# Kernel tuning notes

Measured on AMD Instinct MI355X. Metric: run time of the kernel, lower is better.

Reference implementation:

```python
import jax, jax.numpy as jnp
import numpy as np

N_NODES = 100000
N_EDGES = 1600000
IN_CH = 64
HID = 64
N_LAYERS = 4


def setup_inputs() -> dict:
    key = jax.random.key(0)
    ks = jax.random.split(key, 12)
    x = jax.random.normal(ks[0], (N_NODES, IN_CH), dtype=jnp.float32)
    edge_index = jax.random.randint(ks[1], (2, N_EDGES), 0, N_NODES, dtype=jnp.int64)
    s = 1.0 / np.sqrt(HID)
    W_enc = jax.random.normal(ks[2], (IN_CH, HID), dtype=jnp.float32) * s
    b_enc = jnp.zeros((HID,), dtype=jnp.float32)
    Wg = jax.random.normal(ks[3], (N_LAYERS, HID, HID), dtype=jnp.float32) * s
    bg = jnp.zeros((N_LAYERS, HID), dtype=jnp.float32)
    # MLPReadout: 64 -> 32 -> 16 -> 1
    W0 = jax.random.normal(ks[4], (HID, HID // 2), dtype=jnp.float32) * s
    b0 = jnp.zeros((HID // 2,), dtype=jnp.float32)
    W1 = jax.random.normal(ks[5], (HID // 2, HID // 4), dtype=jnp.float32) * (1.0 / np.sqrt(HID // 2))
    b1 = jnp.zeros((HID // 4,), dtype=jnp.float32)
    W2 = jax.random.normal(ks[6], (HID // 4, 1), dtype=jnp.float32) * (1.0 / np.sqrt(HID // 4))
    b2 = jnp.zeros((1,), dtype=jnp.float32)
    return {"x": x, "edge_index": edge_index, "W_enc": W_enc, "b_enc": b_enc,
            "Wg": Wg, "bg": bg, "W0": W0, "b0": b0, "W1": W1, "b1": b1,
            "W2": W2, "b2": b2}


def _gcn_norm(edge_index, n_nodes):
    # PyG GCNConv default: add self-loops, symmetric normalization.
    loop = jnp.arange(n_nodes, dtype=edge_index.dtype)
    src = jnp.concatenate([edge_index[0], loop])  # [E + N]
    dst = jnp.concatenate([edge_index[1], loop])
    deg = jax.ops.segment_sum(jnp.ones_like(dst, dtype=jnp.float32), dst,
                              num_segments=n_nodes)
    dinv = jnp.where(deg > 0, 1.0 / jnp.sqrt(deg), 0.0)
    norm = dinv[src] * dinv[dst]  # [E + N]
    return src, dst, norm


def reference(x, edge_index, W_enc, b_enc, Wg, bg, W0, b0, W1, b1, W2, b2):
    n_nodes = x.shape[0]
    src, dst, norm = _gcn_norm(edge_index, n_nodes)
    h = x @ W_enc + b_enc  # feature encoder [N, HID]
    n_layers = Wg.shape[0]
    for l in range(n_layers):
        h_res = h
        hw = h @ Wg[l]                                  # [N, HID] GEMM
        msg = hw[src] * norm[:, None]                   # gather + scale
        h = jax.ops.segment_sum(msg, dst, num_segments=n_nodes) + bg[l]
        h = h + h_res                                   # residual
        if l != n_layers - 1:
            # dropout in eval mode is identity
            h = jax.nn.relu(h)
    # MLPReadout (L=2)
    y = jax.nn.relu(h @ W0 + b0)
    y = jax.nn.relu(y @ W1 + b1)
    y = y @ W2 + b2  # [N, 1]
    return y
```

## Files before the change

kernel.cpp:

```cpp
#include <hip/hip_runtime.h>

typedef __attribute__((ext_vector_type(8))) short bf16x8_t;
typedef __attribute__((ext_vector_type(4))) float f32x4_t;

#define PINF(x) asm volatile("" : "+v"(x))


#define PCHUNK 4096
#define PTHREADS 512
#define EPT (PCHUNK / PTHREADS)
#define NBUCK_MAX 400
#define BCAP 6144

__global__ __launch_bounds__(PTHREADS)
void k_partition2(const int* __restrict__ src, const int* __restrict__ dst,
                  int* __restrict__ bcnt, unsigned int* __restrict__ stageg,
                  int E, int nbuck) {
    __shared__ int hist[NBUCK_MAX];
    __shared__ int boffs[NBUCK_MAX];
    __shared__ int cur[NBUCK_MAX];
    __shared__ int gbase[NBUCK_MAX];
    __shared__ int tmp[PTHREADS];
    __shared__ unsigned int stage[PCHUNK];
    __shared__ unsigned short sbid[PCHUNK];

    int tid = threadIdx.x;
    int ebase = blockIdx.x * PCHUNK;
    int ecount = min(PCHUNK, E - ebase);

    if (tid < NBUCK_MAX) hist[tid] = 0;
    __syncthreads();

    int dreg[EPT], sreg[EPT];
#pragma unroll
    for (int k = 0; k < EPT; k++) {
        int e = ebase + tid + k * PTHREADS;
        if (tid + k * PTHREADS < ecount) {
            dreg[k] = dst[e];
            sreg[k] = src[e];
            atomicAdd(&hist[dreg[k] >> 8], 1);
        } else dreg[k] = -1;
    }
    __syncthreads();

    int v = (tid < nbuck) ? hist[tid] : 0;
    tmp[tid] = v;
    __syncthreads();
    for (int d = 1; d < PTHREADS; d <<= 1) {
        int t = (tid >= d) ? tmp[tid - d] : 0;
        __syncthreads();
        tmp[tid] += t;
        __syncthreads();
    }
    if (tid < nbuck) { boffs[tid] = tmp[tid] - v; cur[tid] = tmp[tid] - v; }
    __syncthreads();

#pragma unroll
    for (int k = 0; k < EPT; k++) {
        if (dreg[k] >= 0) {
            int b = dreg[k] >> 8;
            int p = atomicAdd(&cur[b], 1);
            stage[p] = ((unsigned int)(dreg[k] & 255) << 17) | (unsigned int)sreg[k];
            sbid[p] = (unsigned short)b;
        }
    }
    __syncthreads();

    if (tid < nbuck) {
        int c = cur[tid] - boffs[tid];
        if (c > 0) gbase[tid] = atomicAdd(&bcnt[tid], c);
    }
    __syncthreads();

    for (int i = tid; i < ecount; i += PTHREADS) {
        int b = sbid[i];
        stageg[(size_t)b * BCAP + gbase[b] + (i - boffs[b])] = stage[i];
    }
}


__global__ __launch_bounds__(512)
void k_bucket_scan(const int* __restrict__ bcnt, int* __restrict__ bbase, int nbuck) {
    __shared__ int tmp[512];
    int tid = threadIdx.x;
    int v = (tid < nbuck) ? bcnt[tid] : 0;
    tmp[tid] = v;
    __syncthreads();
    for (int d = 1; d < 512; d <<= 1) {
        int t = (tid >= d) ? tmp[tid - d] : 0;
        __syncthreads();
        tmp[tid] += t;
        __syncthreads();
    }
    if (tid < nbuck) bbase[tid] = tmp[tid] - v;
    if (tid == nbuck - 1) bbase[nbuck] = tmp[tid];
}


__global__ __launch_bounds__(1024)
void k_finefill2(const unsigned int* __restrict__ stageg, const int* __restrict__ bcnt,
                 const int* __restrict__ bbase, int* __restrict__ offs,
                 float* __restrict__ dinv, int* __restrict__ col, int N, int nbuck) {
    __shared__ int cnt0[256];
    __shared__ int excl[256];
    __shared__ int cur[256];
    __shared__ unsigned int stage[BCAP];
    int b = blockIdx.x;
    int tid = threadIdx.x;
    int nbase = b << 8;
    int nn = min(256, N - nbase);
    int n = bcnt[b];
    int base = bbase[b];
    const unsigned int* sg = stageg + (size_t)b * BCAP;

    if (tid < 256) cnt0[tid] = 0;
    __syncthreads();

    for (int i = tid; i < n; i += 1024)
        atomicAdd(&cnt0[sg[i] >> 17], 1);
    __syncthreads();

    if (tid < 256) excl[tid] = cnt0[tid];
    __syncthreads();
    for (int d = 1; d < 256; d <<= 1) {
        int t = 0;
        if (tid < 256 && tid >= d) t = excl[tid - d];
        __syncthreads();
        if (tid < 256) excl[tid] += t;
        __syncthreads();
    }
    if (tid < 256) {
        int e = excl[tid] - cnt0[tid];
        cur[tid] = e;
        if (tid < nn) {
            offs[nbase + tid] = base + e;
            dinv[nbase + tid] = rsqrtf((float)(cnt0[tid] + 1));
        }
    }
    if (b == nbuck - 1 && tid == 0) offs[N] = bbase[nbuck];
    __syncthreads();

    for (int i = tid; i < n; i += 1024) {
        unsigned int v = sg[i];
        int p = atomicAdd(&cur[v >> 17], 1);
        stage[p] = v & 0x1FFFFu;
    }
    __syncthreads();
    for (int i = tid; i < n; i += 1024)
        col[base + i] = (int)stage[i];
}


__device__ __forceinline__ unsigned int bf16rne(float x) {
    unsigned int u = __float_as_uint(x);
    return (u + 0x7FFFu + ((u >> 16) & 1u)) >> 16;
}
__device__ __forceinline__ float u2flo(unsigned int u) { return __uint_as_float(u << 16); }
__device__ __forceinline__ float u2fhi(unsigned int u) { return __uint_as_float(u & 0xFFFF0000u); }

__device__ __forceinline__ void split2(float a, float b, unsigned int& hi, unsigned int& lo) {
    unsigned int ha = bf16rne(a), hb = bf16rne(b);
    float ra = a - u2flo(ha), rb = b - u2flo(hb);
    hi = ha | (hb << 16);
    lo = bf16rne(ra) | (bf16rne(rb) << 16);
}

union FragU { uint4 u4; bf16x8_t bf; };


__global__ __launch_bounds__(256)
void k_wsplit(const float* __restrict__ Wenc, const float* __restrict__ Wg,
              unsigned int* __restrict__ wfragg, int* __restrict__ bcnt) {
    int m = blockIdx.x;
    int tid = threadIdx.x;
    if (m == 0 && tid < 256) { bcnt[tid] = 0; bcnt[tid + 256] = 0; }
    const float* W = (m == 0) ? Wenc : (Wg + (size_t)(m - 1) * 4096);
    unsigned int* wb = wfragg + (size_t)m * 4096;
#pragma unroll
    for (int i = 0; i < 16; i++) {
        int flat = tid * 16 + i;
        int mm = flat & 3;
        int l = (flat >> 2) & 63;
        int fp = flat >> 8;
        int p = fp & 1;
        int f = fp >> 1;
        int ct = f >> 1, kh = f & 1;
        int k = kh * 32 + ((l >> 4) << 3) + 2 * mm;
        int c = ct * 16 + (l & 15);
        float w0 = W[k * 64 + c];
        float w1 = W[(k + 1) * 64 + c];
        unsigned int hi, lo;
        split2(w0, w1, hi, lo);
        wb[flat] = p ? lo : hi;
    }
}


__global__ __launch_bounds__(256)
void k_enc_fused(const float* __restrict__ x, const uint4* __restrict__ wfE,
                 const float* __restrict__ benc, const uint4* __restrict__ wfG,
                 const float* __restrict__ dinv, float* __restrict__ h,
                 unsigned short* __restrict__ hwb_out, int N) {
    __shared__ float hlds[64 * 68];

    int tid = threadIdx.x;
    int lane = tid & 63;
    int w = tid >> 6;
    int rowbase = blockIdx.x * 64 + w * 16;

    FragU ahi[2], alo[2];
    {
        int row = rowbase + (lane & 15);
        int rc = min(row, N - 1);
#pragma unroll
        for (int kh = 0; kh < 2; kh++) {
            const float4* hp = (const float4*)(x + (size_t)rc * 64 + kh * 32 + ((lane >> 4) << 3));
            float4 p0 = hp[0], p1 = hp[1];
            split2(p0.x, p0.y, ahi[kh].u4.x, alo[kh].u4.x);
            split2(p0.z, p0.w, ahi[kh].u4.y, alo[kh].u4.y);
            split2(p1.x, p1.y, ahi[kh].u4.z, alo[kh].u4.z);
            split2(p1.z, p1.w, ahi[kh].u4.w, alo[kh].u4.w);
        }
    }

    f32x4_t acc[4];
#pragma unroll
    for (int ct = 0; ct < 4; ct++) {
        float b = benc[ct * 16 + (lane & 15)];
        acc[ct] = (f32x4_t){b, b, b, b};
    }
#pragma unroll
    for (int ct = 0; ct < 4; ct++) {
#pragma unroll
        for (int kh = 0; kh < 2; kh++) {
            FragU bhi, blo;
            bhi.u4 = wfE[((ct * 2 + kh) * 2 + 0) * 64 + lane];
            blo.u4 = wfE[((ct * 2 + kh) * 2 + 1) * 64 + lane];
            acc[ct] = __builtin_amdgcn_mfma_f32_16x16x32_bf16(ahi[kh].bf, bhi.bf, acc[ct], 0, 0, 0);
            acc[ct] = __builtin_amdgcn_mfma_f32_16x16x32_bf16(alo[kh].bf, bhi.bf, acc[ct], 0, 0, 0);
            acc[ct] = __builtin_amdgcn_mfma_f32_16x16x32_bf16(ahi[kh].bf, blo.bf, acc[ct], 0, 0, 0);
        }
    }

    float dv[4];
#pragma unroll
    for (int r = 0; r < 4; r++) {
        int row = rowbase + ((lane >> 4) << 2) + r;
        dv[r] = dinv[min(row, N - 1)];
    }
#pragma unroll
    for (int ct = 0; ct < 4; ct++) {
#pragma unroll
        for (int r = 0; r < 4; r++) {
            int row = rowbase + ((lane >> 4) << 2) + r;
            float v = acc[ct][r];
            if (row < N) h[(size_t)row * 64 + ct * 16 + (lane & 15)] = v;
            hlds[(w * 16 + ((lane >> 4) << 2) + r) * 68 + ct * 16 + (lane & 15)] = v * dv[r];
        }
    }
    __syncthreads();

    FragU a2hi[2], a2lo[2];
#pragma unroll
    for (int kh = 0; kh < 2; kh++) {
        const float4* hp = (const float4*)(hlds + (w * 16 + (lane & 15)) * 68 + kh * 32 + ((lane >> 4) << 3));
        float4 p0 = hp[0], p1 = hp[1];
        split2(p0.x, p0.y, a2hi[kh].u4.x, a2lo[kh].u4.x);
        split2(p0.z, p0.w, a2hi[kh].u4.y, a2lo[kh].u4.y);
        split2(p1.x, p1.y, a2hi[kh].u4.z, a2lo[kh].u4.z);
        split2(p1.z, p1.w, a2hi[kh].u4.w, a2lo[kh].u4.w);
    }

#pragma unroll
    for (int ct = 0; ct < 4; ct++) {
        f32x4_t a2 = (f32x4_t){0.f, 0.f, 0.f, 0.f};
#pragma unroll
        for (int kh = 0; kh < 2; kh++) {
            FragU bhi, blo;
            bhi.u4 = wfG[((ct * 2 + kh) * 2 + 0) * 64 + lane];
            blo.u4 = wfG[((ct * 2 + kh) * 2 + 1) * 64 + lane];
            a2 = __builtin_amdgcn_mfma_f32_16x16x32_bf16(a2hi[kh].bf, bhi.bf, a2, 0, 0, 0);
            a2 = __builtin_amdgcn_mfma_f32_16x16x32_bf16(a2lo[kh].bf, bhi.bf, a2, 0, 0, 0);
            a2 = __builtin_amdgcn_mfma_f32_16x16x32_bf16(a2hi[kh].bf, blo.bf, a2, 0, 0, 0);
        }
#pragma unroll
        for (int r = 0; r < 4; r++) {
            float v = a2[r];
            float vo = __shfl_xor(v, 1);
            int row = rowbase + ((lane >> 4) << 2) + r;
            if (!(lane & 1) && row < N) {
                unsigned int pk = bf16rne(v) | (bf16rne(vo) << 16);
                *(unsigned int*)(hwb_out + (size_t)row * 64 + ct * 16 + (lane & 15)) = pk;
            }
        }
    }
}


__global__ __launch_bounds__(256, 4)
void k_agg_fused(const unsigned short* __restrict__ hwb_in, const int* __restrict__ offs,
                 const int* __restrict__ col, const float* __restrict__ dinv,
                 const float* __restrict__ bg, float* __restrict__ h,
                 const uint4* __restrict__ wnext, unsigned short* __restrict__ hwb_out,
                 int N) {
    __shared__ uint4 wlds[16 * 64];

    int tid = threadIdx.x;
#pragma unroll
    for (int i = 0; i < 4; i++)
        wlds[tid + i * 256] = wnext[tid + i * 256];
    __syncthreads();

    int t = blockIdx.x * 256 + tid;
    int wid = t >> 6;
    int lane = tid & 63;
    int G = lane >> 3;
    int L = lane & 7;
    int node = wid * 8 + G;
    bool valid = node < N;
    int nc = valid ? node : N - 1;

    int start = offs[nc];
    int end = valid ? offs[nc + 1] : start;

    float dn = dinv[nc];
    float* hrow = h + (size_t)nc * 64 + L * 8;
    float4 hr0 = ((const float4*)hrow)[0];
    float4 hr1 = ((const float4*)hrow)[1];
    const float* bgp = bg + L * 8;
    float bs0 = bgp[0] + hr0.x, bs1 = bgp[1] + hr0.y, bs2 = bgp[2] + hr0.z, bs3 = bgp[3] + hr0.w;
    float bs4 = bgp[4] + hr1.x, bs5 = bgp[5] + hr1.y, bs6 = bgp[6] + hr1.z, bs7 = bgp[7] + hr1.w;
    PINF(bs0); PINF(bs1); PINF(bs2); PINF(bs3);
    PINF(bs4); PINF(bs5); PINF(bs6); PINF(bs7); PINF(dn);

    uint4 v = ((const uint4*)(hwb_in + (size_t)nc * 64))[L];
    float a0 = u2flo(v.x), a1 = u2fhi(v.x);
    float a2 = u2flo(v.y), a3 = u2fhi(v.y);
    float a4 = u2flo(v.z), a5 = u2fhi(v.z);
    float a6 = u2flo(v.w), a7 = u2fhi(v.w);

    int last = (end > start) ? (end - 1) : 0;
    int e = start;
    int cc0 = col[min(e + 0, last)];
    int cc1 = col[min(e + 1, last)];
    int cc2 = col[min(e + 2, last)];
    int cc3 = col[min(e + 3, last)];
    for (;;) {
        bool act0 = e < end;
        if (__ballot(act0) == 0ULL) break;
        bool act1 = e + 1 < end, act2 = e + 2 < end, act3 = e + 3 < end;
        uint4 v0 = ((const uint4*)(hwb_in + (size_t)cc0 * 64))[L];
        uint4 v1 = ((const uint4*)(hwb_in + (size_t)cc1 * 64))[L];
        uint4 v2 = ((const uint4*)(hwb_in + (size_t)cc2 * 64))[L];
        uint4 v3 = ((const uint4*)(hwb_in + (size_t)cc3 * 64))[L];
        int en = e + 4;
        cc0 = col[min(en + 0, last)];
        cc1 = col[min(en + 1, last)];
        cc2 = col[min(en + 2, last)];
        cc3 = col[min(en + 3, last)];
        if (!act0) { v0.x = 0u; v0.y = 0u; v0.z = 0u; v0.w = 0u; }
        if (!act1) { v1.x = 0u; v1.y = 0u; v1.z = 0u; v1.w = 0u; }
        if (!act2) { v2.x = 0u; v2.y = 0u; v2.z = 0u; v2.w = 0u; }
        if (!act3) { v3.x = 0u; v3.y = 0u; v3.z = 0u; v3.w = 0u; }
        a0 += (u2flo(v0.x) + u2flo(v1.x)) + (u2flo(v2.x) + u2flo(v3.x));
        a1 += (u2fhi(v0.x) + u2fhi(v1.x)) + (u2fhi(v2.x) + u2fhi(v3.x));
        a2 += (u2flo(v0.y) + u2flo(v1.y)) + (u2flo(v2.y) + u2flo(v3.y));
        a3 += (u2fhi(v0.y) + u2fhi(v1.y)) + (u2fhi(v2.y) + u2fhi(v3.y));
        a4 += (u2flo(v0.z) + u2flo(v1.z)) + (u2flo(v2.z) + u2flo(v3.z));
        a5 += (u2fhi(v0.z) + u2fhi(v1.z)) + (u2fhi(v2.z) + u2fhi(v3.z));
        a6 += (u2flo(v0.w) + u2flo(v1.w)) + (u2flo(v2.w) + u2flo(v3.w));
        a7 += (u2fhi(v0.w) + u2fhi(v1.w)) + (u2fhi(v2.w) + u2fhi(v3.w));
        e = en;
    }

    float4 o0, o1;
    o0.x = fmaxf(fmaf(dn, a0, bs0), 0.f);
    o0.y = fmaxf(fmaf(dn, a1, bs1), 0.f);
    o0.z = fmaxf(fmaf(dn, a2, bs2), 0.f);
    o0.w = fmaxf(fmaf(dn, a3, bs3), 0.f);
    o1.x = fmaxf(fmaf(dn, a4, bs4), 0.f);
    o1.y = fmaxf(fmaf(dn, a5, bs5), 0.f);
    o1.z = fmaxf(fmaf(dn, a6, bs6), 0.f);
    o1.w = fmaxf(fmaf(dn, a7, bs7), 0.f);
    if (valid) {
        ((float4*)hrow)[0] = o0;
        ((float4*)hrow)[1] = o1;
    }

    float sv0 = o0.x * dn, sv1 = o0.y * dn, sv2 = o0.z * dn, sv3 = o0.w * dn;
    float sv4 = o1.x * dn, sv5 = o1.y * dn, sv6 = o1.z * dn, sv7 = o1.w * dn;

    int r = lane & 15;
    int kb = lane >> 4;
    int srcA = (r & 7) * 8 + kb;
    int srcB = (r & 7) * 8 + 4 + kb;

    FragU ahi0, alo0, ahi1, alo1;
    {
        float c0 = __shfl(sv0, srcA), c1 = __shfl(sv1, srcA);
        float c2 = __shfl(sv2, srcA), c3 = __shfl(sv3, srcA);
        float c4 = __shfl(sv4, srcA), c5 = __shfl(sv5, srcA);
        float c6 = __shfl(sv6, srcA), c7 = __shfl(sv7, srcA);
        split2(c0, c1, ahi0.u4.x, alo0.u4.x);
        split2(c2, c3, ahi0.u4.y, alo0.u4.y);
        split2(c4, c5, ahi0.u4.z, alo0.u4.z);
        split2(c6, c7, ahi0.u4.w, alo0.u4.w);
    }
    {
        float c0 = __shfl(sv0, srcB), c1 = __shfl(sv1, srcB);
        float c2 = __shfl(sv2, srcB), c3 = __shfl(sv3, srcB);
        float c4 = __shfl(sv4, srcB), c5 = __shfl(sv5, srcB);
        float c6 = __shfl(sv6, srcB), c7 = __shfl(sv7, srcB);
        split2(c0, c1, ahi1.u4.x, alo1.u4.x);
        split2(c2, c3, ahi1.u4.y, alo1.u4.y);
        split2(c4, c5, ahi1.u4.z, alo1.u4.z);
        split2(c6, c7, ahi1.u4.w, alo1.u4.w);
    }

    f32x4_t acc[4];
#pragma unroll
    for (int ct = 0; ct < 4; ct++) acc[ct] = (f32x4_t){0.f, 0.f, 0.f, 0.f};

#pragma unroll
    for (int ct = 0; ct < 4; ct++) {
        FragU bh0, bl0, bh1, bl1;
        bh0.u4 = wlds[((ct * 2 + 0) * 2 + 0) * 64 + lane];
        bl0.u4 = wlds[((ct * 2 + 0) * 2 + 1) * 64 + lane];
        bh1.u4 = wlds[((ct * 2 + 1) * 2 + 0) * 64 + lane];
        bl1.u4 = wlds[((ct * 2 + 1) * 2 + 1) * 64 + lane];
        acc[ct] = __builtin_amdgcn_mfma_f32_16x16x32_bf16(ahi0.bf, bh0.bf, acc[ct], 0, 0, 0);
        acc[ct] = __builtin_amdgcn_mfma_f32_16x16x32_bf16(alo0.bf, bh0.bf, acc[ct], 0, 0, 0);
        acc[ct] = __builtin_amdgcn_mfma_f32_16x16x32_bf16(ahi0.bf, bl0.bf, acc[ct], 0, 0, 0);
        acc[ct] = __builtin_amdgcn_mfma_f32_16x16x32_bf16(ahi1.bf, bh1.bf, acc[ct], 0, 0, 0);
        acc[ct] = __builtin_amdgcn_mfma_f32_16x16x32_bf16(alo1.bf, bh1.bf, acc[ct], 0, 0, 0);
        acc[ct] = __builtin_amdgcn_mfma_f32_16x16x32_bf16(ahi1.bf, bl1.bf, acc[ct], 0, 0, 0);
    }

    int wbase = wid * 8;
#pragma unroll
    for (int ct = 0; ct < 4; ct++) {
#pragma unroll
        for (int rr = 0; rr < 4; rr++) {
            float vv = acc[ct][rr];
            float vo = __shfl_xor(vv, 1);
            int orow = ((lane >> 4) << 2) + rr;
            int onode = wbase + orow;
            if (!(lane & 1) && orow < 8 && onode < N) {
                unsigned int pk = bf16rne(vv) | (bf16rne(vo) << 16);
                *(unsigned int*)(hwb_out + (size_t)onode * 64 + ct * 16 + (lane & 15)) = pk;
            }
        }
    }
}


__global__ __launch_bounds__(256)
void k_agg(const unsigned short* __restrict__ hwb, const int* __restrict__ offs,
           const int* __restrict__ col, const float* __restrict__ dinv,
           const float* __restrict__ bg, float* __restrict__ h, int N) {
    int t = blockIdx.x * blockDim.x + threadIdx.x;
    int wid = t >> 6;
    int lane = threadIdx.x & 63;
    int G = lane >> 3;
    int L = lane & 7;
    int node = wid * 8 + G;
    bool valid = node < N;
    int nc = valid ? node : N - 1;

    int start = offs[nc];
    int end = valid ? offs[nc + 1] : start;

    float dn = dinv[nc];
    float* hrow = h + (size_t)nc * 64 + L * 8;
    float4 hr0 = ((const float4*)hrow)[0];
    float4 hr1 = ((const float4*)hrow)[1];
    const float* bgp = bg + L * 8;
    float bs0 = bgp[0] + hr0.x, bs1 = bgp[1] + hr0.y, bs2 = bgp[2] + hr0.z, bs3 = bgp[3] + hr0.w;
    float bs4 = bgp[4] + hr1.x, bs5 = bgp[5] + hr1.y, bs6 = bgp[6] + hr1.z, bs7 = bgp[7] + hr1.w;
    PINF(bs0); PINF(bs1); PINF(bs2); PINF(bs3);
    PINF(bs4); PINF(bs5); PINF(bs6); PINF(bs7); PINF(dn);

    uint4 v = ((const uint4*)(hwb + (size_t)nc * 64))[L];
    float a0 = u2flo(v.x), a1 = u2fhi(v.x);
    float a2 = u2flo(v.y), a3 = u2fhi(v.y);
    float a4 = u2flo(v.z), a5 = u2fhi(v.z);
    float a6 = u2flo(v.w), a7 = u2fhi(v.w);

    int last = (end > start) ? (end - 1) : 0;
    int e = start;
    int cc0 = col[min(e + 0, last)];
    int cc1 = col[min(e + 1, last)];
    int cc2 = col[min(e + 2, last)];
    int cc3 = col[min(e + 3, last)];
    for (;;) {
        bool act0 = e < end;
        if (__ballot(act0) == 0ULL) break;
        bool act1 = e + 1 < end, act2 = e + 2 < end, act3 = e + 3 < end;
        uint4 v0 = ((const uint4*)(hwb + (size_t)cc0 * 64))[L];
        uint4 v1 = ((const uint4*)(hwb + (size_t)cc1 * 64))[L];
        uint4 v2 = ((const uint4*)(hwb + (size_t)cc2 * 64))[L];
        uint4 v3 = ((const uint4*)(hwb + (size_t)cc3 * 64))[L];
        int en = e + 4;
        cc0 = col[min(en + 0, last)];
        cc1 = col[min(en + 1, last)];
        cc2 = col[min(en + 2, last)];
        cc3 = col[min(en + 3, last)];
        if (!act0) { v0.x = 0u; v0.y = 0u; v0.z = 0u; v0.w = 0u; }
        if (!act1) { v1.x = 0u; v1.y = 0u; v1.z = 0u; v1.w = 0u; }
        if (!act2) { v2.x = 0u; v2.y = 0u; v2.z = 0u; v2.w = 0u; }
        if (!act3) { v3.x = 0u; v3.y = 0u; v3.z = 0u; v3.w = 0u; }
        a0 += (u2flo(v0.x) + u2flo(v1.x)) + (u2flo(v2.x) + u2flo(v3.x));
        a1 += (u2fhi(v0.x) + u2fhi(v1.x)) + (u2fhi(v2.x) + u2fhi(v3.x));
        a2 += (u2flo(v0.y) + u2flo(v1.y)) + (u2flo(v2.y) + u2flo(v3.y));
        a3 += (u2fhi(v0.y) + u2fhi(v1.y)) + (u2fhi(v2.y) + u2fhi(v3.y));
        a4 += (u2flo(v0.z) + u2flo(v1.z)) + (u2flo(v2.z) + u2flo(v3.z));
        a5 += (u2fhi(v0.z) + u2fhi(v1.z)) + (u2fhi(v2.z) + u2fhi(v3.z));
        a6 += (u2flo(v0.w) + u2flo(v1.w)) + (u2flo(v2.w) + u2flo(v3.w));
        a7 += (u2fhi(v0.w) + u2fhi(v1.w)) + (u2fhi(v2.w) + u2fhi(v3.w));
        e = en;
    }

    if (valid) {
        float4 o0, o1;
        o0.x = fmaf(dn, a0, bs0);
        o0.y = fmaf(dn, a1, bs1);
        o0.z = fmaf(dn, a2, bs2);
        o0.w = fmaf(dn, a3, bs3);
        o1.x = fmaf(dn, a4, bs4);
        o1.y = fmaf(dn, a5, bs5);
        o1.z = fmaf(dn, a6, bs6);
        o1.w = fmaf(dn, a7, bs7);
        ((float4*)hrow)[0] = o0;
        ((float4*)hrow)[1] = o1;
    }
}


__global__ __launch_bounds__(256)
void k_readout(const float* __restrict__ h,
               const float* __restrict__ W0, const float* __restrict__ b0,
               const float* __restrict__ W1, const float* __restrict__ b1,
               const float* __restrict__ W2, const float* __restrict__ b2,
               float* __restrict__ out, int N) {
    int r = blockIdx.x * 256 + threadIdx.x;
    if (r >= N) return;

    float t0[32];
#pragma unroll
    for (int c = 0; c < 32; c++) t0[c] = b0[c];

    const float4* h4 = (const float4*)(h + (size_t)r * 64);
#pragma unroll
    for (int k4 = 0; k4 < 16; k4++) {
        float4 v = h4[k4];
#pragma unroll
        for (int kk = 0; kk < 4; kk++) {
            float xk = (kk == 0) ? v.x : (kk == 1) ? v.y : (kk == 2) ? v.z : v.w;
            const float* wr = W0 + (k4 * 4 + kk) * 32;
#pragma unroll
            for (int c = 0; c < 32; c++) t0[c] = fmaf(xk, wr[c], t0[c]);
        }
    }
#pragma unroll
    for (int c = 0; c < 32; c++) t0[c] = fmaxf(t0[c], 0.f);

    float t1[16];
#pragma unroll
    for (int c = 0; c < 16; c++) t1[c] = b1[c];
#pragma unroll
    for (int k = 0; k < 32; k++) {
        const float* wr = W1 + k * 16;
#pragma unroll
        for (int c = 0; c < 16; c++) t1[c] = fmaf(t0[k], wr[c], t1[c]);
    }
#pragma unroll
    for (int c = 0; c < 16; c++) t1[c] = fmaxf(t1[c], 0.f);

    float y = b2[0];
#pragma unroll
    for (int k = 0; k < 16; k++) y = fmaf(t1[k], W2[k], y);
    out[r] = y;
}


extern "C" void kernel_launch(void* const* d_in, const int* in_sizes, int n_in,
                              void* d_out, int out_size, void* d_ws, size_t ws_size,
                              hipStream_t stream) {
    const float* x     = (const float*)d_in[0];
    const int*   eidx  = (const int*)d_in[1];
    const float* W_enc = (const float*)d_in[2];
    const float* b_enc = (const float*)d_in[3];
    const float* Wg    = (const float*)d_in[4];
    const float* bg    = (const float*)d_in[5];
    const float* W0    = (const float*)d_in[6];
    const float* b0    = (const float*)d_in[7];
    const float* W1    = (const float*)d_in[8];
    const float* b1    = (const float*)d_in[9];
    const float* W2    = (const float*)d_in[10];
    const float* b2    = (const float*)d_in[11];

    int N = in_sizes[0] / 64;
    int E = in_sizes[1] / 2;
    const int* esrc = eidx;
    const int* edst = eidx + E;
    int nbuck = (N + 255) >> 8;

    char* w = (char*)d_ws;
    auto alloc = [&](size_t bytes) -> char* {
        char* p = w;
        w += (bytes + 255) & ~(size_t)255;
        return p;
    };
    int*   bcnt  = (int*)alloc(512 * 4);
    int*   bbase = (int*)alloc(512 * 4);
    int*   offs  = (int*)alloc((size_t)(N + 1) * 4);
    int*   col   = (int*)alloc((size_t)E * 4);
    unsigned int* stageg = (unsigned int*)alloc((size_t)nbuck * BCAP * 4);
    float* dinv  = (float*)alloc((size_t)N * 4);
    float* h     = (float*)alloc((size_t)N * 64 * 4);
    unsigned short* hwbA = (unsigned short*)alloc((size_t)N * 64 * 2);
    unsigned short* hwbB = (unsigned short*)alloc((size_t)N * 64 * 2);
    unsigned int* wfragg = (unsigned int*)alloc(5 * 4096 * 4);

    k_wsplit<<<5, 256, 0, stream>>>(W_enc, Wg, wfragg, bcnt);
    k_partition2<<<(E + PCHUNK - 1) / PCHUNK, PTHREADS, 0, stream>>>(esrc, edst, bcnt, stageg, E, nbuck);
    k_bucket_scan<<<1, 512, 0, stream>>>(bcnt, bbase, nbuck);
    k_finefill2<<<nbuck, 1024, 0, stream>>>(stageg, bcnt, bbase, offs, dinv, col, N, nbuck);

    int gbE = (N + 63) / 64;
    int gb = (N + 255) / 256;
    int aggthreads = ((N + 7) / 8) * 64;
    int aggblocks = (aggthreads + 255) / 256;

    k_enc_fused<<<gbE, 256, 0, stream>>>(
        x, (const uint4*)wfragg, b_enc, (const uint4*)(wfragg + (size_t)1 * 4096),
        dinv, h, hwbA, N);
    k_agg_fused<<<aggblocks, 256, 0, stream>>>(hwbA, offs, col, dinv, bg + 0 * 64, h,
                                               (const uint4*)(wfragg + (size_t)2 * 4096), hwbB, N);
    k_agg_fused<<<aggblocks, 256, 0, stream>>>(hwbB, offs, col, dinv, bg + 1 * 64, h,
                                               (const uint4*)(wfragg + (size_t)3 * 4096), hwbA, N);
    k_agg_fused<<<aggblocks, 256, 0, stream>>>(hwbA, offs, col, dinv, bg + 2 * 64, h,
                                               (const uint4*)(wfragg + (size_t)4 * 4096), hwbB, N);
    k_agg<<<aggblocks, 256, 0, stream>>>(hwbB, offs, col, dinv, bg + 3 * 64, h, N);
    k_readout<<<gb, 256, 0, stream>>>(h, W0, b0, W1, b1, W2, b2, (float*)d_out, N);
}
```

Measured before the change: 241.1 us.

## Fuse final aggregation layer with MLP readout via cross-lane shuffle reductions

The last GCN aggregation kernel now computes the MLP readout directly instead of writing h back and launching a separate readout kernel. Each 8-lane group splits the 64-wide first layer across lanes and combines the partial sums with xor shuffles. It then splits the 16-wide second layer two outputs per lane and reduces the final dot product with shuffles. This removes one kernel launch and a full write plus reread of the N×64 fp32 h buffer, at the cost of about 96 extra shuffles per lane and more register pressure in the gather kernel.

Result: slower. 296.9 us (+23.1%).

```diff
diff --git a/kernel.cpp b/kernel.cpp
--- a/kernel.cpp
+++ b/kernel.cpp
@@ -455,9 +455,13 @@
 
 
 __global__ __launch_bounds__(256)
-void k_agg(const unsigned short* __restrict__ hwb, const int* __restrict__ offs,
-           const int* __restrict__ col, const float* __restrict__ dinv,
-           const float* __restrict__ bg, float* __restrict__ h, int N) {
+void k_agg_out(const unsigned short* __restrict__ hwb, const int* __restrict__ offs,
+               const int* __restrict__ col, const float* __restrict__ dinv,
+               const float* __restrict__ bg, const float* __restrict__ h,
+               const float* __restrict__ W0, const float* __restrict__ b0,
+               const float* __restrict__ W1, const float* __restrict__ b1,
+               const float* __restrict__ W2, const float* __restrict__ b2,
+               float* __restrict__ out, int N) {
     int t = blockIdx.x * blockDim.x + threadIdx.x;
     int wid = t >> 6;
     int lane = threadIdx.x & 63;
@@ -471,7 +475,7 @@
     int end = valid ? offs[nc + 1] : start;
 
     float dn = dinv[nc];
-    float* hrow = h + (size_t)nc * 64 + L * 8;
+    const float* hrow = h + (size_t)nc * 64 + L * 8;
     float4 hr0 = ((const float4*)hrow)[0];
     float4 hr1 = ((const float4*)hrow)[1];
     const float* bgp = bg + L * 8;
@@ -520,66 +524,49 @@
         e = en;
     }
 
-    if (valid) {
-        float4 o0, o1;
-        o0.x = fmaf(dn, a0, bs0);
-        o0.y = fmaf(dn, a1, bs1);
-        o0.z = fmaf(dn, a2, bs2);
-        o0.w = fmaf(dn, a3, bs3);
-        o1.x = fmaf(dn, a4, bs4);
-        o1.y = fmaf(dn, a5, bs5);
-        o1.z = fmaf(dn, a6, bs6);
-        o1.w = fmaf(dn, a7, bs7);
-        ((float4*)hrow)[0] = o0;
-        ((float4*)hrow)[1] = o1;
-    }
-}
-
-
-__global__ __launch_bounds__(256)
-void k_readout(const float* __restrict__ h,
-               const float* __restrict__ W0, const float* __restrict__ b0,
-               const float* __restrict__ W1, const float* __restrict__ b1,
-               const float* __restrict__ W2, const float* __restrict__ b2,
-               float* __restrict__ out, int N) {
-    int r = blockIdx.x * 256 + threadIdx.x;
-    if (r >= N) return;
+    float hk0 = fmaf(dn, a0, bs0);
+    float hk1 = fmaf(dn, a1, bs1);
+    float hk2 = fmaf(dn, a2, bs2);
+    float hk3 = fmaf(dn, a3, bs3);
+    float hk4 = fmaf(dn, a4, bs4);
+    float hk5 = fmaf(dn, a5, bs5);
+    float hk6 = fmaf(dn, a6, bs6);
+    float hk7 = fmaf(dn, a7, bs7);
 
     float t0[32];
 #pragma unroll
-    for (int c = 0; c < 32; c++) t0[c] = b0[c];
-
-    const float4* h4 = (const float4*)(h + (size_t)r * 64);
-#pragma unroll
-    for (int k4 = 0; k4 < 16; k4++) {
-        float4 v = h4[k4];
-#pragma unroll
-        for (int kk = 0; kk < 4; kk++) {
-            float xk = (kk == 0) ? v.x : (kk == 1) ? v.y : (kk == 2) ? v.z : v.w;
-            const float* wr = W0 + (k4 * 4 + kk) * 32;
-#pragma unroll
-            for (int c = 0; c < 32; c++) t0[c] = fmaf(xk, wr[c], t0[c]);
-        }
+    for (int c = 0; c < 32; c++) t0[c] = (L == 0) ? b0[c] : 0.f;
+    const float* w0p = W0 + (L * 8) * 32;
+#pragma unroll
+    for (int k = 0; k < 8; k++) {
+        float xk = (k == 0) ? hk0 : (k == 1) ? hk1 : (k == 2) ? hk2 : (k == 3) ? hk3
+                 : (k == 4) ? hk4 : (k == 5) ? hk5 : (k == 6) ? hk6 : hk7;
+        const float* wr = w0p + k * 32;
+#pragma unroll
+        for (int c = 0; c < 32; c++) t0[c] = fmaf(xk, wr[c], t0[c]);
+    }
+#pragma unroll
+    for (int m = 1; m <= 4; m <<= 1) {
+#pragma unroll
+        for (int c = 0; c < 32; c++) t0[c] += __shfl_xor(t0[c], m);
     }
 #pragma unroll
     for (int c = 0; c < 32; c++) t0[c] = fmaxf(t0[c], 0.f);
 
-    float t1[16];
-#pragma unroll
-    for (int c = 0; c < 16; c++) t1[c] = b1[c];
+    float t1a = b1[L * 2], t1b = b1[L * 2 + 1];
 #pragma unroll
     for (int k = 0; k < 32; k++) {
-        const float* wr = W1 + k * 16;
-#pragma unroll
-        for (int c = 0; c < 16; c++) t1[c] = fmaf(t0[k], wr[c], t1[c]);
-    }
-#pragma unroll
-    for (int c = 0; c < 16; c++) t1[c] = fmaxf(t1[c], 0.f);
-
-    float y = b2[0];
-#pragma unroll
-    for (int k = 0; k < 16; k++) y = fmaf(t1[k], W2[k], y);
-    out[r] = y;
+        t1a = fmaf(t0[k], W1[k * 16 + L * 2], t1a);
+        t1b = fmaf(t0[k], W1[k * 16 + L * 2 + 1], t1b);
+    }
+    t1a = fmaxf(t1a, 0.f);
+    t1b = fmaxf(t1b, 0.f);
+
+    float y = t1a * W2[L * 2] + t1b * W2[L * 2 + 1];
+#pragma unroll
+    for (int m = 1; m <= 4; m <<= 1) y += __shfl_xor(y, m);
+
+    if (valid && L == 0) out[node] = y + b2[0];
 }
 
 
@@ -628,7 +615,6 @@
     k_finefill2<<<nbuck, 1024, 0, stream>>>(stageg, bcnt, bbase, offs, dinv, col, N, nbuck);
 
     int gbE = (N + 63) / 64;
-    int gb = (N + 255) / 256;
     int aggthreads = ((N + 7) / 8) * 64;
     int aggblocks = (aggthreads + 255) / 256;
 
@@ -641,6 +627,6 @@
                                                (const uint4*)(wfragg + (size_t)3 * 4096), hwbA, N);
     k_agg_fused<<<aggblocks, 256, 0, stream>>>(hwbA, offs, col, dinv, bg + 2 * 64, h,
                                                (const uint4*)(wfragg + (size_t)4 * 4096), hwbB, N);
-    k_agg<<<aggblocks, 256, 0, stream>>>(hwbB, offs, col, dinv, bg + 3 * 64, h, N);
-    k_readout<<<gb, 256, 0, stream>>>(h, W0, b0, W1, b1, W2, b2, (float*)d_out, N);
-}
+    k_agg_out<<<aggblocks, 256, 0, stream>>>(hwbB, offs, col, dinv, bg + 3 * 64, h,
+                                             W0, b0, W1, b1, W2, b2, (float*)d_out, N);
+}
```
